# Kernel tuning notes

Measured on AMD Instinct MI355X. Metric: run time of the kernel, lower is better.

## Reference

```python
import jax, jax.numpy as jnp
import numpy as np

N, L, H, D_HEAD, P = 2, 1024, 8, 64, 1
DIM = H * D_HEAD


def setup_inputs() -> dict:
    key0 = jax.random.key(0)
    ks = jax.random.split(key0, 7)
    query = jax.random.normal(ks[0], (N, L, DIM), dtype=jnp.float32)
    key = jax.random.normal(ks[1], (N, L, DIM), dtype=jnp.float32)
    scale = 1.0 / np.sqrt(DIM)
    Wq = jax.random.normal(ks[2], (DIM, DIM), dtype=jnp.float32) * scale
    Wk = jax.random.normal(ks[3], (DIM, DIM), dtype=jnp.float32) * scale
    Wv = jax.random.normal(ks[4], (DIM, DIM), dtype=jnp.float32) * scale
    position_weight = jax.random.uniform(ks[5], (H, P, D_HEAD), dtype=jnp.float32) * 2 - 1
    position_bias = jax.random.uniform(ks[6], (H, D_HEAD), dtype=jnp.float32) * 2 - 1
    return {"query": query, "key": key, "Wq": Wq, "Wk": Wk, "Wv": Wv,
            "position_weight": position_weight, "position_bias": position_bias}


def _kernel_fn(x):
    # _log_exp_kernel: positive feature map log(1 + exp(x)) (softplus)
    return jax.nn.softplus(x)


def _causal_term(qf, kf, v):
    """Linear-complexity causal attention term.
    qf, kf: (N,H,L,d) feature-mapped query/key; v: (N,H,L,d) values.
    Returns numerator (N,H,L,d) and denominator (N,H,L)."""
    # cumulative key-value outer products: (N,H,L,d,d)
    kv = jnp.cumsum(jnp.einsum('nhkd,nhke->nhkde', kf, v), axis=2)
    num = jnp.einsum('nhqd,nhqde->nhqe', qf, kv)
    den = jnp.einsum('nhqd,nhqd->nhq', qf, jnp.cumsum(kf, axis=2))
    return num, den


def reference(query, key, Wq, Wk, Wv, position_weight, position_bias):
    n, lq, dim = query.shape
    lk = key.shape[1]
    h, p, d = position_weight.shape
    kernel = _kernel_fn
    # projections (torch Linear: x @ W.T), reshape to heads, transpose to (N,H,L,d)
    q = kernel((query @ Wq.T).reshape(n, lq, h, d)).transpose(0, 2, 1, 3)
    k = kernel((key @ Wk.T).reshape(n, lk, h, d)).transpose(0, 2, 1, 3)
    v = ((key @ Wv.T).reshape(n, lk, h, d)).transpose(0, 2, 1, 3)
    # default positions: arange, expanded to (N,L,P)
    qpos = jnp.broadcast_to(jnp.arange(lq, dtype=query.dtype)[None, :, None], (n, lq, p))
    kpos = jnp.broadcast_to(jnp.arange(lk, dtype=key.dtype)[None, :, None], (n, lk, p))
    pq = jnp.einsum('nlp,hpd->nhld', qpos, position_weight) \
         + jax.nn.sigmoid(position_bias)[None, :, None, :] * jnp.pi
    pk = jnp.einsum('nlp,hpd->nhld', kpos, position_weight)
    # three branches: cos, sin, plain (trig identity split of cos(pq - pk) RPE)
    num_c, den_c = _causal_term(q * jnp.cos(pq), k * jnp.cos(pk), v)
    num_s, den_s = _causal_term(q * jnp.sin(pq), k * jnp.sin(pk), v)
    num_p, den_p = _causal_term(q, k, v)
    num = num_c + num_s + num_p
    den = den_c + den_s + den_p
    attention = num / den[..., None]  # scaled=True
    return attention.transpose(0, 2, 1, 3).reshape(n, lq, dim)
```

## Files before the change

### kernel.cpp

```cpp
#include <hip/hip_runtime.h>
#include <hip/hip_bf16.h>

#define LSEQ   1024
#define NHEAD  8
#define DH     64
#define DIM    512
#define NHTOT  16
#define DF     192
#define LDB    68
#define LDQ    200
#define LDV    72

typedef __attribute__((ext_vector_type(8))) short short8;
typedef __attribute__((ext_vector_type(4))) float floatx4;

__device__ __forceinline__ float softplusf_(float x) {
    if (x > 20.f) return x;
    return log1pf(expf(x));
}
__device__ __forceinline__ unsigned short bf16_rne(float x) {
    unsigned int u = __float_as_uint(x);
    u += 0x7FFFu + ((u >> 16) & 1u);
    return (unsigned short)(u >> 16);
}
__device__ __forceinline__ float bf16_tof(unsigned short h) {
    return __uint_as_float(((unsigned int)h) << 16);
}

__global__ __launch_bounds__(256) void proj_kernel(
    const float* __restrict__ query, const float* __restrict__ key,
    const float* __restrict__ Wq, const float* __restrict__ Wk,
    const float* __restrict__ Wv,
    const float* __restrict__ pw, const float* __restrict__ pb,
    unsigned short* __restrict__ qf, unsigned short* __restrict__ kf,
    unsigned short* __restrict__ vbuf)
{
    const int mt  = blockIdx.x;
    const int ot  = blockIdx.y;
    const int sel = blockIdx.z;
    const int t   = threadIdx.x;

    const float* __restrict__ X = (sel == 0) ? query : key;
    const float* __restrict__ W = (sel == 0) ? Wq : (sel == 1) ? Wk : Wv;

    __shared__ unsigned short As[64 * LDB];
    __shared__ unsigned short Bs[64 * LDB];

    const int m0 = mt * 64, o0 = ot * 64;
    const int lane = t & 63, wave = t >> 6;
    const int quad = lane >> 4, l16 = lane & 15;
    const int wm = wave >> 1, wn = wave & 1;

    const int srow = t >> 2;
    const int sc16 = (t & 3) * 16;

    floatx4 acc[2][2];
    #pragma unroll
    for (int i = 0; i < 2; ++i)
        #pragma unroll
        for (int j = 0; j < 2; ++j) acc[i][j] = (floatx4){0.f, 0.f, 0.f, 0.f};

    float4 ax[4], bx4[4];
    #pragma unroll
    for (int i = 0; i < 4; ++i) {
        ax[i]  = *(const float4*)&X[(size_t)(m0 + srow) * DIM + sc16 + i * 4];
        bx4[i] = *(const float4*)&W[(size_t)(o0 + srow) * DIM + sc16 + i * 4];
    }

    for (int kt = 0; kt < DIM; kt += 64) {
        __syncthreads();
        {
            short8 a0, a1, b0, b1;
            #pragma unroll
            for (int i = 0; i < 2; ++i) {
                const float va[4] = {ax[i].x, ax[i].y, ax[i].z, ax[i].w};
                const float vb[4] = {bx4[i].x, bx4[i].y, bx4[i].z, bx4[i].w};
                #pragma unroll
                for (int j = 0; j < 4; ++j) {
                    a0[i * 4 + j] = (short)bf16_rne(va[j]);
                    b0[i * 4 + j] = (short)bf16_rne(vb[j]);
                }
            }
            #pragma unroll
            for (int i = 2; i < 4; ++i) {
                const float va[4] = {ax[i].x, ax[i].y, ax[i].z, ax[i].w};
                const float vb[4] = {bx4[i].x, bx4[i].y, bx4[i].z, bx4[i].w};
                #pragma unroll
                for (int j = 0; j < 4; ++j) {
                    a1[(i - 2) * 4 + j] = (short)bf16_rne(va[j]);
                    b1[(i - 2) * 4 + j] = (short)bf16_rne(vb[j]);
                }
            }
            *(short8*)&As[srow * LDB + sc16]     = a0;
            *(short8*)&As[srow * LDB + sc16 + 8] = a1;
            *(short8*)&Bs[srow * LDB + sc16]     = b0;
            *(short8*)&Bs[srow * LDB + sc16 + 8] = b1;
        }
        __syncthreads();

        if (kt + 64 < DIM) {
            #pragma unroll
            for (int i = 0; i < 4; ++i) {
                ax[i]  = *(const float4*)&X[(size_t)(m0 + srow) * DIM + kt + 64 + sc16 + i * 4];
                bx4[i] = *(const float4*)&W[(size_t)(o0 + srow) * DIM + kt + 64 + sc16 + i * 4];
            }
        }

        #pragma unroll
        for (int s = 0; s < 2; ++s) {
            short8 af[2], bf[2];
            #pragma unroll
            for (int mi = 0; mi < 2; ++mi)
                af[mi] = *(const short8*)&As[(wm * 32 + mi * 16 + l16) * LDB + s * 32 + quad * 8];
            #pragma unroll
            for (int ni = 0; ni < 2; ++ni)
                bf[ni] = *(const short8*)&Bs[(wn * 32 + ni * 16 + l16) * LDB + s * 32 + quad * 8];
            #pragma unroll
            for (int ni = 0; ni < 2; ++ni)
                #pragma unroll
                for (int mi = 0; mi < 2; ++mi)
                    acc[mi][ni] = __builtin_amdgcn_mfma_f32_16x16x32_bf16(af[mi], bf[ni], acc[mi][ni], 0, 0, 0);
        }
    }

    const int h = ot;
    const float PI_ = 3.14159265358979323846f;
    if (sel == 2) {
        #pragma unroll
        for (int mi = 0; mi < 2; ++mi)
            #pragma unroll
            for (int ni = 0; ni < 2; ++ni) {
                const int d = wn * 32 + ni * 16 + l16;
                #pragma unroll
                for (int r = 0; r < 4; ++r) {
                    const int m = m0 + wm * 32 + mi * 16 + quad * 4 + r;
                    const int n = m >> 10, l = m & (LSEQ - 1);
                    vbuf[(((size_t)(n * NHEAD + h)) * LSEQ + l) * DH + d] =
                        bf16_rne(acc[mi][ni][r]);
                }
            }
    } else {
        unsigned short* __restrict__ obuf = (sel == 0) ? qf : kf;
        #pragma unroll
        for (int ni = 0; ni < 2; ++ni) {
            const int d = wn * 32 + ni * 16 + l16;
            const float w = pw[h * DH + d];
            const float bias = (sel == 0) ? PI_ / (1.f + expf(-pb[h * DH + d])) : 0.f;
            #pragma unroll
            for (int mi = 0; mi < 2; ++mi)
                #pragma unroll
                for (int r = 0; r < 4; ++r) {
                    const int m = m0 + wm * 32 + mi * 16 + quad * 4 + r;
                    const int n = m >> 10, l = m & (LSEQ - 1);
                    const float val = softplusf_(acc[mi][ni][r]);
                    float sn, cs;
                    sincosf((float)l * w + bias, &sn, &cs);
                    const size_t ob = (((size_t)(n * NHEAD + h)) * LSEQ + l) * DF + d;
                    obuf[ob]            = bf16_rne(val);
                    obuf[ob + DH]       = bf16_rne(val * cs);
                    obuf[ob + 2 * DH]   = bf16_rne(val * sn);
                }
        }
    }
}

__global__ __launch_bounds__(256) void attn_kernel(
    const unsigned short* __restrict__ qf, const unsigned short* __restrict__ kf,
    const unsigned short* __restrict__ vbuf,
    float* __restrict__ outp)
{
    const int p  = blockIdx.x;
    const int nh = blockIdx.y;
    const int z  = blockIdx.z;
    const int lt = z ? (31 - p) : p;
    const int n  = nh >> 3;
    const int h  = nh & (NHEAD - 1);
    const int t  = threadIdx.x;
    const int lane = t & 63, wave = t >> 6;
    const int quad = lane >> 4, l16 = lane & 15;
    const int wm = wave >> 1, wn = wave & 1;

    __shared__ unsigned short qL[32 * LDQ];
    __shared__ unsigned short kL[64 * LDQ];
    __shared__ unsigned short vT[64 * LDV];
    __shared__ unsigned short scA[32 * LDV];
    __shared__ float denL[2][32];
    __shared__ float inv32[32];

    const size_t fbase = (size_t)nh * LSEQ;
    const int nkt = (lt >> 1) + 1;
    const int diag_kt = lt >> 1;

    #pragma unroll
    for (int i = 0; i < 6; ++i) {
        const int idx = i * 256 + t;
        const int r = idx / 48, c4 = (idx % 48) * 4;
        *(ushort4*)&qL[r * LDQ + c4] =
            *(const ushort4*)&qf[(fbase + lt * 32 + r) * DF + c4];
    }

    floatx4 accN[2];
    accN[0] = (floatx4){0.f, 0.f, 0.f, 0.f};
    accN[1] = (floatx4){0.f, 0.f, 0.f, 0.f};
    float den4[4] = {0.f, 0.f, 0.f, 0.f};

    for (int kt = 0; kt < nkt; ++kt) {
        #pragma unroll
        for (int i = 0; i < 12; ++i) {
            const int idx = i * 256 + t;
            const int r = idx / 48, c4 = (idx % 48) * 4;
            *(ushort4*)&kL[r * LDQ + c4] =
                *(const ushort4*)&kf[(fbase + kt * 64 + r) * DF + c4];
        }
        {
            const int col = t & 63, kq = (t >> 6) * 16;
            unsigned short vvv[16];
            #pragma unroll
            for (int j = 0; j < 16; ++j)
                vvv[j] = vbuf[(fbase + kt * 64 + kq + j) * DH + col];
            #pragma unroll
            for (int g = 0; g < 4; ++g) {
                ushort4 b;
                b.x = vvv[g * 4]; b.y = vvv[g * 4 + 1];
                b.z = vvv[g * 4 + 2]; b.w = vvv[g * 4 + 3];
                *(ushort4*)&vT[col * LDV + kq + g * 4] = b;
            }
        }
        __syncthreads();

        floatx4 accS[2];
        accS[0] = (floatx4){0.f, 0.f, 0.f, 0.f};
        accS[1] = (floatx4){0.f, 0.f, 0.f, 0.f};
        #pragma unroll
        for (int kk = 0; kk < 6; ++kk) {
            const short8 a = *(const short8*)&qL[(wm * 16 + l16) * LDQ + kk * 32 + quad * 8];
            #pragma unroll
            for (int ni = 0; ni < 2; ++ni) {
                const short8 b = *(const short8*)&kL[(wn * 32 + ni * 16 + l16) * LDQ + kk * 32 + quad * 8];
                accS[ni] = __builtin_amdgcn_mfma_f32_16x16x32_bf16(a, b, accS[ni], 0, 0, 0);
            }
        }

        const bool diag = (kt == diag_kt);
        #pragma unroll
        for (int ni = 0; ni < 2; ++ni) {
            const int kcolL = wn * 32 + ni * 16 + l16;
            const int kcolG = kt * 64 + kcolL;
            #pragma unroll
            for (int r = 0; r < 4; ++r) {
                const int lrowL = wm * 16 + quad * 4 + r;
                float sval = accS[ni][r];
                if (diag && kcolG > lt * 32 + lrowL) sval = 0.f;
                den4[r] += sval;
                scA[lrowL * LDV + kcolL] = bf16_rne(sval);
            }
        }
        __syncthreads();

        #pragma unroll
        for (int kk = 0; kk < 2; ++kk) {
            const short8 a = *(const short8*)&scA[(wm * 16 + l16) * LDV + kk * 32 + quad * 8];
            #pragma unroll
            for (int ni = 0; ni < 2; ++ni) {
                const short8 b = *(const short8*)&vT[(wn * 32 + ni * 16 + l16) * LDV + kk * 32 + quad * 8];
                accN[ni] = __builtin_amdgcn_mfma_f32_16x16x32_bf16(a, b, accN[ni], 0, 0, 0);
            }
        }
        __syncthreads();
    }

    #pragma unroll
    for (int r = 0; r < 4; ++r) {
        float s = den4[r];
        s += __shfl_xor(s, 1);
        s += __shfl_xor(s, 2);
        s += __shfl_xor(s, 4);
        s += __shfl_xor(s, 8);
        if (l16 == 0) denL[wn][wm * 16 + quad * 4 + r] = s;
    }
    __syncthreads();
    if (t < 32) inv32[t] = 1.f / (denL[0][t] + denL[1][t]);
    __syncthreads();

    #pragma unroll
    for (int ni = 0; ni < 2; ++ni) {
        const int e = wn * 32 + ni * 16 + l16;
        #pragma unroll
        for (int r = 0; r < 4; ++r) {
            const int row = wm * 16 + quad * 4 + r;
            outp[((size_t)n * LSEQ + lt * 32 + row) * DIM + h * DH + e] =
                accN[ni][r] * inv32[row];
        }
    }
}

extern "C" void kernel_launch(void* const* d_in, const int* in_sizes, int n_in,
                              void* d_out, int out_size, void* d_ws, size_t ws_size,
                              hipStream_t stream) {
    const float* query = (const float*)d_in[0];
    const float* key   = (const float*)d_in[1];
    const float* Wq    = (const float*)d_in[2];
    const float* Wk    = (const float*)d_in[3];
    const float* Wv    = (const float*)d_in[4];
    const float* pw    = (const float*)d_in[5];
    const float* pb    = (const float*)d_in[6];

    unsigned short* U = (unsigned short*)d_ws;
    unsigned short* qf   = U;
    unsigned short* kf   = U + 3145728;
    unsigned short* vbuf = U + 6291456;

    proj_kernel<<<dim3(32, 8, 3), 256, 0, stream>>>(
        query, key, Wq, Wk, Wv, pw, pb, qf, kf, vbuf);
    attn_kernel<<<dim3(16, 16, 2), 256, 0, stream>>>(
        qf, kf, vbuf, (float*)d_out);
}
```

Baseline: 118.9 us.

## Prefetch next K/V tile into registers while computing current tile

```diff
diff --git a/kernel.cpp b/kernel.cpp
--- a/kernel.cpp
+++ b/kernel.cpp
@@ -191,6 +191,15 @@
     const int nkt = (lt >> 1) + 1;
     const int diag_kt = lt >> 1;
 
+    int krr[12], kcc[12];
+    #pragma unroll
+    for (int i = 0; i < 12; ++i) {
+        const int idx = i * 256 + t;
+        krr[i] = idx / 48;
+        kcc[i] = (idx % 48) * 4;
+    }
+    const int vcol = t & 63, vkq = (t >> 6) * 16;
+
     #pragma unroll
     for (int i = 0; i < 6; ++i) {
         const int idx = i * 256 + t;
@@ -198,6 +207,24 @@
         *(ushort4*)&qL[r * LDQ + c4] =
             *(const ushort4*)&qf[(fbase + lt * 32 + r) * DF + c4];
     }
+    #pragma unroll
+    for (int i = 0; i < 12; ++i)
+        *(ushort4*)&kL[krr[i] * LDQ + kcc[i]] =
+            *(const ushort4*)&kf[(fbase + krr[i]) * DF + kcc[i]];
+    {
+        unsigned short vvv[16];
+        #pragma unroll
+        for (int j = 0; j < 16; ++j)
+            vvv[j] = vbuf[(fbase + vkq + j) * DH + vcol];
+        #pragma unroll
+        for (int g = 0; g < 4; ++g) {
+            ushort4 b;
+            b.x = vvv[g * 4]; b.y = vvv[g * 4 + 1];
+            b.z = vvv[g * 4 + 2]; b.w = vvv[g * 4 + 3];
+            *(ushort4*)&vT[vcol * LDV + vkq + g * 4] = b;
+        }
+    }
+    __syncthreads();
 
     floatx4 accN[2];
     accN[0] = (floatx4){0.f, 0.f, 0.f, 0.f};
@@ -205,28 +232,18 @@
     float den4[4] = {0.f, 0.f, 0.f, 0.f};
 
     for (int kt = 0; kt < nkt; ++kt) {
-        #pragma unroll
-        for (int i = 0; i < 12; ++i) {
-            const int idx = i * 256 + t;
-            const int r = idx / 48, c4 = (idx % 48) * 4;
-            *(ushort4*)&kL[r * LDQ + c4] =
-                *(const ushort4*)&kf[(fbase + kt * 64 + r) * DF + c4];
-        }
-        {
-            const int col = t & 63, kq = (t >> 6) * 16;
-            unsigned short vvv[16];
+        ushort4 pk[12];
+        unsigned short pv[16];
+        const bool more = (kt + 1 < nkt);
+        if (more) {
+            const size_t nb = fbase + (size_t)(kt + 1) * 64;
+            #pragma unroll
+            for (int i = 0; i < 12; ++i)
+                pk[i] = *(const ushort4*)&kf[(nb + krr[i]) * DF + kcc[i]];
             #pragma unroll
             for (int j = 0; j < 16; ++j)
-                vvv[j] = vbuf[(fbase + kt * 64 + kq + j) * DH + col];
-            #pragma unroll
-            for (int g = 0; g < 4; ++g) {
-                ushort4 b;
-                b.x = vvv[g * 4]; b.y = vvv[g * 4 + 1];
-                b.z = vvv[g * 4 + 2]; b.w = vvv[g * 4 + 3];
-                *(ushort4*)&vT[col * LDV + kq + g * 4] = b;
-            }
-        }
-        __syncthreads();
+                pv[j] = vbuf[(nb + vkq + j) * DH + vcol];
+        }
 
         floatx4 accS[2];
         accS[0] = (floatx4){0.f, 0.f, 0.f, 0.f};
@@ -267,6 +284,20 @@
             }
         }
         __syncthreads();
+
+        if (more) {
+            #pragma unroll
+            for (int i = 0; i < 12; ++i)
+                *(ushort4*)&kL[krr[i] * LDQ + kcc[i]] = pk[i];
+            #pragma unroll
+            for (int g = 0; g < 4; ++g) {
+                ushort4 b;
+                b.x = pv[g * 4]; b.y = pv[g * 4 + 1];
+                b.z = pv[g * 4 + 2]; b.w = pv[g * 4 + 3];
+                *(ushort4*)&vT[vcol * LDV + vkq + g * 4] = b;
+            }
+            __syncthreads();
+        }
     }
 
     #pragma unroll
```

Result: no change. 119.8 us (+0.8%).
